# Kernel optimization log

Hardware: AMD Instinct MI355X
Metric: run time of the kernel (lower is better)

## Reference

```python
import jax, jax.numpy as jnp
import numpy as np

N = 100000      # nodes
E = 1600000     # edges
F_IN = 128      # num_feat
H = 128         # hidden_dim
EMB = 64        # node_embedding_dim
HL = 256        # hidden_dim_linear


def setup_inputs() -> dict:
    key = jax.random.key(0)
    ks = jax.random.split(key, 12)
    def w(k, fan_in, shape):
        return jax.random.normal(k, shape, dtype=jnp.float32) / np.sqrt(fan_in)
    x = jax.random.normal(ks[0], (N, F_IN), dtype=jnp.float32)
    edge_index = jax.random.randint(ks[1], (2, E), 0, N, dtype=jnp.int32)
    return {
        "x": x,
        "edge_index": edge_index,
        "W0": w(ks[2], F_IN, (F_IN, H)), "b0": jnp.zeros((H,), jnp.float32),
        "W1": w(ks[3], H, (H, H)),       "b1": jnp.zeros((H,), jnp.float32),
        "W2": w(ks[4], H, (H, EMB)),     "b2": jnp.zeros((EMB,), jnp.float32),
        "lw1": w(ks[5], 2 * EMB, (2 * EMB, HL)), "lb1": jnp.zeros((HL,), jnp.float32),
        "lw2": w(ks[6], HL, (HL, 1)),            "lb2": jnp.zeros((1,), jnp.float32),
    }


def _gcn_forward(x, edge_index, W0, b0, W1, b1, W2, b2, lw1, lb1, lw2, lb2):
    src, dst = edge_index[0], edge_index[1]
    # add self loops (PyG GCNConv default) -- shared across layers
    loop = jnp.arange(N, dtype=src.dtype)
    s = jnp.concatenate([src, loop])
    d = jnp.concatenate([dst, loop])
    # symmetric normalization: deg counts incoming edges incl. self loop (>=1)
    deg = jax.ops.segment_sum(jnp.ones_like(d, dtype=x.dtype), d, num_segments=N)
    norm = jax.lax.rsqrt(deg[s] * deg[d])  # [E+N]

    def conv(h, W, b):
        hw = h @ W                                   # small GEMM [N, out]
        msg = hw[s] * norm[:, None]                  # gather + scale [E+N, out]
        agg = jax.ops.segment_sum(msg, d, num_segments=N)
        return agg + b

    z = jax.nn.relu(conv(x, W0, b0))
    z = jax.nn.relu(conv(z, W1, b1))
    z = jax.nn.relu(conv(z, W2, b2))                 # [N, EMB]  (dropout: eval mode, no-op)

    # edge classifier: gather both endpoints, cat, MLP, sigmoid
    h = jnp.concatenate([z[src], z[dst]], axis=1)    # [E, 2*EMB]
    h = jax.nn.relu(h @ lw1 + lb1)
    return jax.nn.sigmoid(h @ lw2 + lb2)             # [E, 1]


def reference(x, edge_index, W0, b0, W1, b1, W2, b2, lw1, lb1, lw2, lb2):
    return _gcn_forward(x, edge_index, W0, b0, W1, b1, W2, b2, lw1, lb1, lw2, lb2)
```

## Files before the change

### kernel.cpp

```cpp
#include <hip/hip_runtime.h>

#define NNODES 100000
#define NEDGES 1600000
#define NBLK 391
#define NSLICE 8
#define SLICEW 12500
#define CNTB 6250
#define GB0 1563

typedef __attribute__((ext_vector_type(8))) short bf16x8;
typedef __attribute__((ext_vector_type(4))) float f32x4;

__device__ __forceinline__ unsigned short f2bf(float f) {
  unsigned int u = __float_as_uint(f);
  u = (u + 0x7FFFu + ((u >> 16) & 1u)) >> 16;
  return (unsigned short)u;
}
__device__ __forceinline__ float bf2f(unsigned short h) {
  return __uint_as_float(((unsigned int)h) << 16);
}

__device__ __forceinline__ unsigned int pk_add_f16(unsigned int a, unsigned int b) {
  unsigned int r;
  asm("v_pk_add_f16 %0, %1, %2" : "=v"(r) : "v"(a), "v"(b));
  return r;
}
__device__ __forceinline__ unsigned int pk_max0_f16(unsigned int a, unsigned int z) {
  unsigned int r;
  asm("v_pk_max_f16 %0, %1, %2" : "=v"(r) : "v"(a), "v"(z));
  return r;
}
__device__ __forceinline__ float dot2_f16(unsigned int a, unsigned int b, float c) {
  float r;
  asm("v_dot2_f32_f16 %0, %1, %2, %3" : "=v"(r) : "v"(a), "v"(b), "v"(c));
  return r;
}

__global__ __launch_bounds__(256)
void k1_kernel(const int* __restrict__ dst, int* __restrict__ cntD,
               const float* __restrict__ W0, const float* __restrict__ W1,
               const float* __restrict__ W2, const float* __restrict__ lw1,
               const float* __restrict__ lb1, const float* __restrict__ lw2,
               unsigned short* __restrict__ Wp0, unsigned short* __restrict__ Wp1,
               unsigned short* __restrict__ Wp2, unsigned short* __restrict__ WpE,
               float* __restrict__ biasAB, unsigned int* __restrict__ wh) {
  int b = blockIdx.x;
  int tid = threadIdx.x;
  if (b < CNTB) {
    int e = b * 256 + tid;
    if (e < NEDGES) atomicAdd(&cntD[dst[e]], 1);
    return;
  }
  int bb = b - CNTB;
  if (bb < 64) {
    int idx = bb * 256 + tid;
    int k = idx >> 7, c = idx & 127;
    Wp0[((size_t)((k >> 5) * 128 + c)) * 32 + (k & 31)] = f2bf(W0[idx]);
  } else if (bb < 128) {
    int idx = (bb - 64) * 256 + tid;
    int k = idx >> 7, c = idx & 127;
    Wp1[((size_t)((k >> 5) * 128 + c)) * 32 + (k & 31)] = f2bf(W1[idx]);
  } else if (bb < 160) {
    int idx = (bb - 128) * 256 + tid;
    int k = idx >> 6, c = idx & 63;
    Wp2[((size_t)((k >> 5) * 64 + c)) * 32 + (k & 31)] = f2bf(W2[idx]);
  } else {
    int idx = (bb - 160) * 256 + tid;
    int k = idx >> 9, c = idx & 511;
    float v = (c < 256) ? lw1[k * 256 + c] : lw1[(64 + k) * 256 + (c - 256)];
    WpE[((size_t)((k >> 5) * 512 + c)) * 32 + (k & 31)] = f2bf(v);
    if (idx < 512) biasAB[idx] = (idx < 256) ? lb1[idx] : 0.0f;
    if (idx < 128) {
      _Float16 lo = (_Float16)lw2[idx * 2];
      _Float16 hi = (_Float16)lw2[idx * 2 + 1];
      unsigned short ulo = __builtin_bit_cast(unsigned short, lo);
      unsigned short uhi = __builtin_bit_cast(unsigned short, hi);
      wh[idx] = (unsigned int)ulo | ((unsigned int)uhi << 16);
    }
  }
}

__global__ void scanA_kernel(const int* __restrict__ cntD, int* __restrict__ blockSum,
                             float* __restrict__ dis) {
  __shared__ int sh[256];
  int v = blockIdx.x * 256 + threadIdx.x;
  int c = (v < NNODES) ? cntD[v] : 0;
  if (v < NNODES) dis[v] = rsqrtf((float)(c + 1));
  sh[threadIdx.x] = c;
  __syncthreads();
  for (int off = 128; off; off >>= 1) {
    if (threadIdx.x < off) sh[threadIdx.x] += sh[threadIdx.x + off];
    __syncthreads();
  }
  if (threadIdx.x == 0) blockSum[blockIdx.x] = sh[0];
}

__global__ void scanB_kernel(int* __restrict__ blockSum) {
  int lane = threadIdx.x;
  int carry = 0;
  for (int base = 0; base < NBLK; base += 64) {
    int i = base + lane;
    int c = (i < NBLK) ? blockSum[i] : 0;
    int pre = c;
#pragma unroll
    for (int off = 1; off < 64; off <<= 1) {
      int t = __shfl_up(pre, off);
      if (lane >= off) pre += t;
    }
    int tot = __shfl(pre, 63);
    if (i < NBLK) blockSum[i] = carry + pre - c;
    carry += tot;
  }
}

template <int K, int HOUT, bool SCALE, bool BIAS, bool F32IN, bool F16OUT>
__device__ __forceinline__ void mgemm_body(int bid, const void* __restrict__ Xhi_v,
                                           const void* __restrict__ Xlo_v,
                                           const unsigned short* __restrict__ Wp,
                                           const float* __restrict__ dis,
                                           const float* __restrict__ bias,
                                           void* __restrict__ outv) {
  constexpr int KC = K / 32;
  const int tid = threadIdx.x;
  const int wave = tid >> 6;
  const int lane = tid & 63;
  const int lrow = lane & 15;
  const int lsub = lane >> 4;
  const int rowBase = bid * 64 + wave * 16;
  int arow = rowBase + lrow;
  if (arow > NNODES - 1) arow = NNODES - 1;
  bf16x8 ahi[KC], alo[KC];
  if constexpr (F32IN) {
    const float* xf = (const float*)Xhi_v;
#pragma unroll
    for (int kc = 0; kc < KC; ++kc) {
      float4 v0 = *(const float4*)&xf[(size_t)arow * K + kc * 32 + lsub * 8];
      float4 v1 = *(const float4*)&xf[(size_t)arow * K + kc * 32 + lsub * 8 + 4];
      float fv[8] = {v0.x, v0.y, v0.z, v0.w, v1.x, v1.y, v1.z, v1.w};
#pragma unroll
      for (int i = 0; i < 8; ++i) {
        unsigned short h = f2bf(fv[i]);
        ahi[kc][i] = (short)h;
        alo[kc][i] = (short)f2bf(fv[i] - bf2f(h));
      }
    }
  } else {
    const unsigned short* Xhi = (const unsigned short*)Xhi_v;
    const unsigned short* Xlo = (const unsigned short*)Xlo_v;
#pragma unroll
    for (int kc = 0; kc < KC; ++kc) {
      ahi[kc] = *(const bf16x8*)&Xhi[(size_t)arow * K + kc * 32 + lsub * 8];
      alo[kc] = *(const bf16x8*)&Xlo[(size_t)arow * K + kc * 32 + lsub * 8];
    }
  }
  int orow[4];
  float dis4[4];
#pragma unroll
  for (int i = 0; i < 4; ++i) {
    orow[i] = rowBase + lsub * 4 + i;
    int rc = orow[i] < NNODES ? orow[i] : NNODES - 1;
    dis4[i] = SCALE ? dis[rc] : 1.0f;
  }
  for (int ct = 0; ct < HOUT / 16; ++ct) {
    int c = ct * 16 + lrow;
    f32x4 acc = {0.f, 0.f, 0.f, 0.f};
#pragma unroll
    for (int kc = 0; kc < KC; ++kc) {
      bf16x8 b = *(const bf16x8*)&Wp[((size_t)(kc * HOUT + c)) * 32 + lsub * 8];
      acc = __builtin_amdgcn_mfma_f32_16x16x32_bf16(ahi[kc], b, acc, 0, 0, 0);
      acc = __builtin_amdgcn_mfma_f32_16x16x32_bf16(alo[kc], b, acc, 0, 0, 0);
    }
    float bb = BIAS ? bias[c] : 0.0f;
#pragma unroll
    for (int i = 0; i < 4; ++i) {
      if (orow[i] < NNODES) {
        float v = acc[i];
        if (SCALE) v *= dis4[i];
        if (BIAS) v += bb;
        if constexpr (F16OUT) {
          ((_Float16*)outv)[(size_t)orow[i] * HOUT + c] = (_Float16)v;
        } else {
          ((unsigned short*)outv)[(size_t)orow[i] * HOUT + c] = f2bf(v);
        }
      }
    }
  }
}

template <int K, int HOUT, bool SCALE, bool BIAS, bool F32IN, bool F16OUT>
__global__ __launch_bounds__(256)
void mgemm_kernel(const void* __restrict__ Xhi_v, const void* __restrict__ Xlo_v,
                  const unsigned short* __restrict__ Wp, const float* __restrict__ dis,
                  const float* __restrict__ bias, void* __restrict__ outv) {
  mgemm_body<K, HOUT, SCALE, BIAS, F32IN, F16OUT>(blockIdx.x, Xhi_v, Xlo_v, Wp, dis, bias, outv);
}

__global__ __launch_bounds__(256)
void mg0_scanC_kernel(const float* __restrict__ x, const unsigned short* __restrict__ Wp0,
                      const float* __restrict__ dis, unsigned short* __restrict__ P16,
                      const int* __restrict__ cntD, const int* __restrict__ blockSum,
                      int* __restrict__ startD, int* __restrict__ curD) {
  if (blockIdx.x < GB0) {
    mgemm_body<128, 128, true, false, true, false>(blockIdx.x, x, nullptr, Wp0, dis, nullptr, P16);
    return;
  }
  __shared__ int sh[256];
  int bid = blockIdx.x - GB0;
  int tid = threadIdx.x;
  int v = bid * 256 + tid;
  int c = (v < NNODES) ? cntD[v] : 0;
  sh[tid] = c;
  __syncthreads();
  for (int off = 1; off < 256; off <<= 1) {
    int t = (tid >= off) ? sh[tid - off] : 0;
    __syncthreads();
    sh[tid] += t;
    __syncthreads();
  }
  if (v < NNODES) {
    int s = blockSum[bid] + sh[tid] - c;
    startD[v] = s;
    curD[v] = s;
  }
}

__global__ void fill_kernel(const int* __restrict__ src, const int* __restrict__ dst,
                            int* __restrict__ curD, int2* __restrict__ csrPair) {
  int slice = blockIdx.x & (NSLICE - 1);
  int e = (blockIdx.x >> 3) * 256 + threadIdx.x;
  if (e >= NEDGES) return;
  int d = dst[e];
  int lo = slice * SLICEW;
  if (d < lo || d >= lo + SLICEW) return;
  int s = src[e];
  int pd = atomicAdd(&curD[d], 1);
  csrPair[pd] = make_int2(s, e);
}

template <int HOUT>
__global__ __launch_bounds__(256)
void agg_kernel(const unsigned short* __restrict__ hws, const int2* __restrict__ csrPair,
                const int* __restrict__ startA, const int* __restrict__ cnt,
                const float* __restrict__ dis, const float* __restrict__ bias,
                unsigned short* __restrict__ outHi, unsigned short* __restrict__ outLo) {
  int gid = blockIdx.x * 256 + threadIdx.x;
  int v = gid >> 6;
  int lane = gid & 63;
  constexpr int PER = HOUT / 64;
  float acc0 = 0.0f, acc1 = 0.0f;
  if constexpr (PER == 2) {
    unsigned int o = *(const unsigned int*)&hws[(size_t)v * HOUT + lane * 2];
    acc0 = __uint_as_float(o << 16);
    acc1 = __uint_as_float(o & 0xffff0000u);
  } else {
    acc0 = bf2f(hws[(size_t)v * HOUT + lane]);
  }
  int s0 = startA[v], c = cnt[v];
  for (int base = 0; base < c; base += 64) {
    int rem = c - base;
    int m = rem < 64 ? rem : 64;
    int idx = 0;
    if (lane < m) idx = csrPair[s0 + base + lane].x;
    int j = 0;
    for (; j + 8 <= m; j += 8) {
      int u0 = __shfl(idx, j);
      int u1 = __shfl(idx, j + 1);
      int u2 = __shfl(idx, j + 2);
      int u3 = __shfl(idx, j + 3);
      int u4 = __shfl(idx, j + 4);
      int u5 = __shfl(idx, j + 5);
      int u6 = __shfl(idx, j + 6);
      int u7 = __shfl(idx, j + 7);
      if constexpr (PER == 2) {
        unsigned int r0 = *(const unsigned int*)&hws[(size_t)u0 * HOUT + lane * 2];
        unsigned int r1 = *(const unsigned int*)&hws[(size_t)u1 * HOUT + lane * 2];
        unsigned int r2 = *(const unsigned int*)&hws[(size_t)u2 * HOUT + lane * 2];
        unsigned int r3 = *(const unsigned int*)&hws[(size_t)u3 * HOUT + lane * 2];
        unsigned int r4 = *(const unsigned int*)&hws[(size_t)u4 * HOUT + lane * 2];
        unsigned int r5 = *(const unsigned int*)&hws[(size_t)u5 * HOUT + lane * 2];
        unsigned int r6 = *(const unsigned int*)&hws[(size_t)u6 * HOUT + lane * 2];
        unsigned int r7 = *(const unsigned int*)&hws[(size_t)u7 * HOUT + lane * 2];
        acc0 += (__uint_as_float(r0 << 16) + __uint_as_float(r1 << 16)) +
                (__uint_as_float(r2 << 16) + __uint_as_float(r3 << 16)) +
                (__uint_as_float(r4 << 16) + __uint_as_float(r5 << 16)) +
                (__uint_as_float(r6 << 16) + __uint_as_float(r7 << 16));
        acc1 += (__uint_as_float(r0 & 0xffff0000u) + __uint_as_float(r1 & 0xffff0000u)) +
                (__uint_as_float(r2 & 0xffff0000u) + __uint_as_float(r3 & 0xffff0000u)) +
                (__uint_as_float(r4 & 0xffff0000u) + __uint_as_float(r5 & 0xffff0000u)) +
                (__uint_as_float(r6 & 0xffff0000u) + __uint_as_float(r7 & 0xffff0000u));
      } else {
        float r0 = bf2f(hws[(size_t)u0 * HOUT + lane]);
        float r1 = bf2f(hws[(size_t)u1 * HOUT + lane]);
        float r2 = bf2f(hws[(size_t)u2 * HOUT + lane]);
        float r3 = bf2f(hws[(size_t)u3 * HOUT + lane]);
        float r4 = bf2f(hws[(size_t)u4 * HOUT + lane]);
        float r5 = bf2f(hws[(size_t)u5 * HOUT + lane]);
        float r6 = bf2f(hws[(size_t)u6 * HOUT + lane]);
        float r7 = bf2f(hws[(size_t)u7 * HOUT + lane]);
        acc0 += ((r0 + r1) + (r2 + r3)) + ((r4 + r5) + (r6 + r7));
      }
    }
    for (; j + 4 <= m; j += 4) {
      int u0 = __shfl(idx, j);
      int u1 = __shfl(idx, j + 1);
      int u2 = __shfl(idx, j + 2);
      int u3 = __shfl(idx, j + 3);
      if constexpr (PER == 2) {
        unsigned int r0 = *(const unsigned int*)&hws[(size_t)u0 * HOUT + lane * 2];
        unsigned int r1 = *(const unsigned int*)&hws[(size_t)u1 * HOUT + lane * 2];
        unsigned int r2 = *(const unsigned int*)&hws[(size_t)u2 * HOUT + lane * 2];
        unsigned int r3 = *(const unsigned int*)&hws[(size_t)u3 * HOUT + lane * 2];
        acc0 += __uint_as_float(r0 << 16) + __uint_as_float(r1 << 16) +
                __uint_as_float(r2 << 16) + __uint_as_float(r3 << 16);
        acc1 += __uint_as_float(r0 & 0xffff0000u) + __uint_as_float(r1 & 0xffff0000u) +
                __uint_as_float(r2 & 0xffff0000u) + __uint_as_float(r3 & 0xffff0000u);
      } else {
        float r0 = bf2f(hws[(size_t)u0 * HOUT + lane]);
        float r1 = bf2f(hws[(size_t)u1 * HOUT + lane]);
        float r2 = bf2f(hws[(size_t)u2 * HOUT + lane]);
        float r3 = bf2f(hws[(size_t)u3 * HOUT + lane]);
        acc0 += (r0 + r1) + (r2 + r3);
      }
    }
    for (; j < m; ++j) {
      int u = __shfl(idx, j);
      if constexpr (PER == 2) {
        unsigned int r = *(const unsigned int*)&hws[(size_t)u * HOUT + lane * 2];
        acc0 += __uint_as_float(r << 16);
        acc1 += __uint_as_float(r & 0xffff0000u);
      } else {
        acc0 += bf2f(hws[(size_t)u * HOUT + lane]);
      }
    }
  }
  float d = dis[v];
  if constexpr (PER == 2) {
    float o0 = fmaf(d, acc0, bias[lane * 2]);
    float o1 = fmaf(d, acc1, bias[lane * 2 + 1]);
    o0 = o0 > 0.0f ? o0 : 0.0f;
    o1 = o1 > 0.0f ? o1 : 0.0f;
    ushort2 h, l;
    h.x = f2bf(o0); l.x = f2bf(o0 - bf2f(h.x));
    h.y = f2bf(o1); l.y = f2bf(o1 - bf2f(h.y));
    *(ushort2*)&outHi[(size_t)v * HOUT + lane * 2] = h;
    *(ushort2*)&outLo[(size_t)v * HOUT + lane * 2] = l;
  } else {
    float o0 = fmaf(d, acc0, bias[lane]);
    o0 = o0 > 0.0f ? o0 : 0.0f;
    unsigned short h = f2bf(o0);
    outHi[(size_t)v * HOUT + lane] = h;
    outLo[(size_t)v * HOUT + lane] = f2bf(o0 - bf2f(h));
  }
}

__global__ __launch_bounds__(256)
void edge_kernel(const unsigned int* __restrict__ AB32,
                 const int2* __restrict__ csrPair,
                 const int* __restrict__ startD, const int* __restrict__ cntD,
                 const unsigned int* __restrict__ wh, const float* __restrict__ lb2,
                 float* __restrict__ out) {
  int gid = blockIdx.x * 256 + threadIdx.x;
  int v = gid >> 6;
  int lane = gid & 63;
  int sub = lane & 15;
  unsigned int zero = 0u;
  unsigned int bu[8], wu[8];
  {
    const unsigned int* Brow = AB32 + (size_t)v * 256 + 128 + sub * 8;
    uint4 b0 = *(const uint4*)Brow;
    uint4 b1 = *(const uint4*)(Brow + 4);
    bu[0] = b0.x; bu[1] = b0.y; bu[2] = b0.z; bu[3] = b0.w;
    bu[4] = b1.x; bu[5] = b1.y; bu[6] = b1.z; bu[7] = b1.w;
    const unsigned int* W = wh + sub * 8;
    uint4 w0 = *(const uint4*)W;
    uint4 w1 = *(const uint4*)(W + 4);
    wu[0] = w0.x; wu[1] = w0.y; wu[2] = w0.z; wu[3] = w0.w;
    wu[4] = w1.x; wu[5] = w1.y; wu[6] = w1.z; wu[7] = w1.w;
  }
  float lb = lb2[0];

  int s0 = startD[v], c = cntD[v];
  for (int base = 0; base < c; base += 64) {
    int rem = c - base;
    int m = rem < 64 ? rem : 64;
    int sj = 0, ej = 0;
    if (lane < m) {
      int2 p = csrPair[s0 + base + lane];
      sj = p.x; ej = p.y;
    }
    int g = lane >> 4;
    for (int j = 0; j < m; j += 8) {
      int ls0 = j + g, ls1 = j + 4 + g;
      int l0 = ls0 < m ? ls0 : m - 1;
      int l1 = ls1 < m ? ls1 : m - 1;
      int sA = __shfl(sj, l0);
      int eA = __shfl(ej, l0);
      int sB = __shfl(sj, l1);
      int eB = __shfl(ej, l1);
      const unsigned int* ArowA = AB32 + (size_t)(unsigned)sA * 256 + sub * 8;
      const unsigned int* ArowB = AB32 + (size_t)(unsigned)sB * 256 + sub * 8;
      uint4 a00 = *(const uint4*)ArowA;
      uint4 a01 = *(const uint4*)(ArowA + 4);
      uint4 a10 = *(const uint4*)ArowB;
      uint4 a11 = *(const uint4*)(ArowB + 4);
      unsigned int au0[8] = {a00.x, a00.y, a00.z, a00.w, a01.x, a01.y, a01.z, a01.w};
      unsigned int au1[8] = {a10.x, a10.y, a10.z, a10.w, a11.x, a11.y, a11.z, a11.w};
      float acc0 = 0.f, acc1 = 0.f;
#pragma unroll
      for (int i = 0; i < 8; ++i) {
        unsigned int h0 = pk_max0_f16(pk_add_f16(au0[i], bu[i]), zero);
        acc0 = dot2_f16(h0, wu[i], acc0);
        unsigned int h1 = pk_max0_f16(pk_add_f16(au1[i], bu[i]), zero);
        acc1 = dot2_f16(h1, wu[i], acc1);
      }
      acc0 += __shfl_xor(acc0, 1);
      acc0 += __shfl_xor(acc0, 2);
      acc0 += __shfl_xor(acc0, 4);
      acc0 += __shfl_xor(acc0, 8);
      acc1 += __shfl_xor(acc1, 1);
      acc1 += __shfl_xor(acc1, 2);
      acc1 += __shfl_xor(acc1, 4);
      acc1 += __shfl_xor(acc1, 8);
      if (ls0 < m && sub == 0) out[eA] = 1.0f / (1.0f + expf(-(acc0 + lb)));
      if (ls1 < m && sub == 0) out[eB] = 1.0f / (1.0f + expf(-(acc1 + lb)));
    }
  }
}

extern "C" void kernel_launch(void* const* d_in, const int* in_sizes, int n_in,
                              void* d_out, int out_size, void* d_ws, size_t ws_size,
                              hipStream_t stream) {
  const float* x   = (const float*)d_in[0];
  const int*   ei  = (const int*)d_in[1];
  const float* W0  = (const float*)d_in[2];
  const float* b0  = (const float*)d_in[3];
  const float* W1  = (const float*)d_in[4];
  const float* b1  = (const float*)d_in[5];
  const float* W2  = (const float*)d_in[6];
  const float* b2  = (const float*)d_in[7];
  const float* lw1 = (const float*)d_in[8];
  const float* lb1 = (const float*)d_in[9];
  const float* lw2 = (const float*)d_in[10];
  const float* lb2 = (const float*)d_in[11];
  float* out = (float*)d_out;
  const int* src = ei;
  const int* dst = ei + NEDGES;

  char* ws = (char*)d_ws;
  size_t off = 0;
  auto alloc = [&](size_t bytes) -> void* {
    void* p = ws + off;
    off += (bytes + 255) & ~(size_t)255;
    return p;
  };
  int*   cntD   = (int*)alloc((size_t)NNODES * 4);
  int*   startD = (int*)alloc((size_t)NNODES * 4);
  int*   curD   = (int*)alloc((size_t)NNODES * 4);
  float* dis    = (float*)alloc((size_t)NNODES * 4);
  int*   blockSum = (int*)alloc((size_t)NBLK * 4);
  int2*  csrPair= (int2*)alloc((size_t)NEDGES * 8);
  unsigned short* P16  = (unsigned short*)alloc((size_t)NNODES * 128 * 2);
  unsigned short* XQhi = (unsigned short*)alloc((size_t)NNODES * 128 * 2);
  unsigned short* XQlo = (unsigned short*)alloc((size_t)NNODES * 128 * 2);
  void*           AB   = alloc((size_t)NNODES * 512 * 2);
  unsigned short* Wp0  = (unsigned short*)alloc((size_t)128 * 128 * 2);
  unsigned short* Wp1  = (unsigned short*)alloc((size_t)128 * 128 * 2);
  unsigned short* Wp2  = (unsigned short*)alloc((size_t)128 * 64 * 2);
  unsigned short* WpE  = (unsigned short*)alloc((size_t)64 * 512 * 2);
  float* biasAB = (float*)alloc(512 * 4);
  unsigned int* wh = (unsigned int*)alloc(128 * 4);

  const int EB8 = NSLICE * CNTB;
  const int AB_ = (NNODES * 64) / 256;

  hipMemsetAsync(cntD, 0, (size_t)NNODES * 4, stream);
  k1_kernel<<<CNTB + 288, 256, 0, stream>>>(dst, cntD, W0, W1, W2, lw1, lb1, lw2,
                                            Wp0, Wp1, Wp2, WpE, biasAB, wh);
  scanA_kernel<<<NBLK, 256, 0, stream>>>(cntD, blockSum, dis);
  scanB_kernel<<<1, 64, 0, stream>>>(blockSum);
  mg0_scanC_kernel<<<GB0 + NBLK, 256, 0, stream>>>(x, Wp0, dis, P16, cntD, blockSum, startD, curD);
  fill_kernel<<<EB8, 256, 0, stream>>>(src, dst, curD, csrPair);

  agg_kernel<128><<<AB_, 256, 0, stream>>>(P16, csrPair, startD, cntD, dis, b0, XQhi, XQlo);
  mgemm_kernel<128, 128, true, false, false, false><<<GB0, 256, 0, stream>>>(XQhi, XQlo, Wp1, dis, nullptr, P16);
  agg_kernel<128><<<AB_, 256, 0, stream>>>(P16, csrPair, startD, cntD, dis, b1, XQhi, XQlo);
  mgemm_kernel<128, 64, true, false, false, false><<<GB0, 256, 0, stream>>>(XQhi, XQlo, Wp2, dis, nullptr, P16);
  agg_kernel<64><<<AB_, 256, 0, stream>>>(P16, csrPair, startD, cntD, dis, b2, XQhi, XQlo);

  mgemm_kernel<64, 512, false, true, false, true><<<GB0, 256, 0, stream>>>(XQhi, XQlo, WpE, nullptr, biasAB, AB);

  edge_kernel<<<AB_, 256, 0, stream>>>((const unsigned int*)AB, csrPair, startD, cntD, wh, lb2, out);
}
```

Baseline: 580.8 us.

## Fuse neighbor aggregation with following MFMA GEMM via shared-memory staging

Replaces the separate aggregation and GEMM kernels with one fused kernel per layer. Each 64-node block gathers and reduces neighbor features into shared-memory hi/lo bf16 tiles, then runs the MFMA GEMM directly from LDS. This removes the global write and re-read of the intermediate XQhi/XQlo buffers and three kernel launches. In exchange, each wave now handles 16 nodes sequentially instead of one node per wave, which may reduce latency hiding for the irregular gathers and adds LDS pressure that can lower occupancy.

```diff
diff --git a/kernel.cpp b/kernel.cpp
--- a/kernel.cpp
+++ b/kernel.cpp
@@ -113,6 +113,101 @@
   }
 }
 
+template <int H>
+__device__ __forceinline__ void agg_node(int v, const unsigned short* __restrict__ hws,
+                                         const int2* __restrict__ csrPair,
+                                         const int* __restrict__ startD,
+                                         const int* __restrict__ cntD,
+                                         int lane, float& acc0, float& acc1) {
+  constexpr int PER = H / 64;
+  if constexpr (PER == 2) {
+    unsigned int o = *(const unsigned int*)&hws[(size_t)v * H + lane * 2];
+    acc0 = __uint_as_float(o << 16);
+    acc1 = __uint_as_float(o & 0xffff0000u);
+  } else {
+    acc0 = bf2f(hws[(size_t)v * H + lane]);
+    acc1 = 0.0f;
+  }
+  int s0 = startD[v], c = cntD[v];
+  for (int base = 0; base < c; base += 64) {
+    int rem = c - base;
+    int m = rem < 64 ? rem : 64;
+    int idx = 0;
+    if (lane < m) idx = csrPair[s0 + base + lane].x;
+    int j = 0;
+    for (; j + 8 <= m; j += 8) {
+      int u0 = __shfl(idx, j);
+      int u1 = __shfl(idx, j + 1);
+      int u2 = __shfl(idx, j + 2);
+      int u3 = __shfl(idx, j + 3);
+      int u4 = __shfl(idx, j + 4);
+      int u5 = __shfl(idx, j + 5);
+      int u6 = __shfl(idx, j + 6);
+      int u7 = __shfl(idx, j + 7);
+      if constexpr (PER == 2) {
+        unsigned int r0 = *(const unsigned int*)&hws[(size_t)u0 * H + lane * 2];
+        unsigned int r1 = *(const unsigned int*)&hws[(size_t)u1 * H + lane * 2];
+        unsigned int r2 = *(const unsigned int*)&hws[(size_t)u2 * H + lane * 2];
+        unsigned int r3 = *(const unsigned int*)&hws[(size_t)u3 * H + lane * 2];
+        unsigned int r4 = *(const unsigned int*)&hws[(size_t)u4 * H + lane * 2];
+        unsigned int r5 = *(const unsigned int*)&hws[(size_t)u5 * H + lane * 2];
+        unsigned int r6 = *(const unsigned int*)&hws[(size_t)u6 * H + lane * 2];
+        unsigned int r7 = *(const unsigned int*)&hws[(size_t)u7 * H + lane * 2];
+        acc0 += (__uint_as_float(r0 << 16) + __uint_as_float(r1 << 16)) +
+                (__uint_as_float(r2 << 16) + __uint_as_float(r3 << 16)) +
+                (__uint_as_float(r4 << 16) + __uint_as_float(r5 << 16)) +
+                (__uint_as_float(r6 << 16) + __uint_as_float(r7 << 16));
+        acc1 += (__uint_as_float(r0 & 0xffff0000u) + __uint_as_float(r1 & 0xffff0000u)) +
+                (__uint_as_float(r2 & 0xffff0000u) + __uint_as_float(r3 & 0xffff0000u)) +
+                (__uint_as_float(r4 & 0xffff0000u) + __uint_as_float(r5 & 0xffff0000u)) +
+                (__uint_as_float(r6 & 0xffff0000u) + __uint_as_float(r7 & 0xffff0000u));
+      } else {
+        float r0 = bf2f(hws[(size_t)u0 * H + lane]);
+        float r1 = bf2f(hws[(size_t)u1 * H + lane]);
+        float r2 = bf2f(hws[(size_t)u2 * H + lane]);
+        float r3 = bf2f(hws[(size_t)u3 * H + lane]);
+        float r4 = bf2f(hws[(size_t)u4 * H + lane]);
+        float r5 = bf2f(hws[(size_t)u5 * H + lane]);
+        float r6 = bf2f(hws[(size_t)u6 * H + lane]);
+        float r7 = bf2f(hws[(size_t)u7 * H + lane]);
+        acc0 += ((r0 + r1) + (r2 + r3)) + ((r4 + r5) + (r6 + r7));
+      }
+    }
+    for (; j + 4 <= m; j += 4) {
+      int u0 = __shfl(idx, j);
+      int u1 = __shfl(idx, j + 1);
+      int u2 = __shfl(idx, j + 2);
+      int u3 = __shfl(idx, j + 3);
+      if constexpr (PER == 2) {
+        unsigned int r0 = *(const unsigned int*)&hws[(size_t)u0 * H + lane * 2];
+        unsigned int r1 = *(const unsigned int*)&hws[(size_t)u1 * H + lane * 2];
+        unsigned int r2 = *(const unsigned int*)&hws[(size_t)u2 * H + lane * 2];
+        unsigned int r3 = *(const unsigned int*)&hws[(size_t)u3 * H + lane * 2];
+        acc0 += __uint_as_float(r0 << 16) + __uint_as_float(r1 << 16) +
+                __uint_as_float(r2 << 16) + __uint_as_float(r3 << 16);
+        acc1 += __uint_as_float(r0 & 0xffff0000u) + __uint_as_float(r1 & 0xffff0000u) +
+                __uint_as_float(r2 & 0xffff0000u) + __uint_as_float(r3 & 0xffff0000u);
+      } else {
+        float r0 = bf2f(hws[(size_t)u0 * H + lane]);
+        float r1 = bf2f(hws[(size_t)u1 * H + lane]);
+        float r2 = bf2f(hws[(size_t)u2 * H + lane]);
+        float r3 = bf2f(hws[(size_t)u3 * H + lane]);
+        acc0 += (r0 + r1) + (r2 + r3);
+      }
+    }
+    for (; j < m; ++j) {
+      int u = __shfl(idx, j);
+      if constexpr (PER == 2) {
+        unsigned int r = *(const unsigned int*)&hws[(size_t)u * H + lane * 2];
+        acc0 += __uint_as_float(r << 16);
+        acc1 += __uint_as_float(r & 0xffff0000u);
+      } else {
+        acc0 += bf2f(hws[(size_t)u * H + lane]);
+      }
+    }
+  }
+}
+
 template <int K, int HOUT, bool SCALE, bool BIAS, bool F32IN, bool F16OUT>
 __device__ __forceinline__ void mgemm_body(int bid, const void* __restrict__ Xhi_v,
                                            const void* __restrict__ Xlo_v,
@@ -187,14 +282,6 @@
   }
 }
 
-template <int K, int HOUT, bool SCALE, bool BIAS, bool F32IN, bool F16OUT>
-__global__ __launch_bounds__(256)
-void mgemm_kernel(const void* __restrict__ Xhi_v, const void* __restrict__ Xlo_v,
-                  const unsigned short* __restrict__ Wp, const float* __restrict__ dis,
-                  const float* __restrict__ bias, void* __restrict__ outv) {
-  mgemm_body<K, HOUT, SCALE, BIAS, F32IN, F16OUT>(blockIdx.x, Xhi_v, Xlo_v, Wp, dis, bias, outv);
-}
-
 __global__ __launch_bounds__(256)
 void mg0_scanC_kernel(const float* __restrict__ x, const unsigned short* __restrict__ Wp0,
                       const float* __restrict__ dis, unsigned short* __restrict__ P16,
@@ -237,119 +324,90 @@
   csrPair[pd] = make_int2(s, e);
 }
 
-template <int HOUT>
+template <int H, int HOUT2, bool SCALE2, bool BIAS2, bool F16OUT2>
 __global__ __launch_bounds__(256)
-void agg_kernel(const unsigned short* __restrict__ hws, const int2* __restrict__ csrPair,
-                const int* __restrict__ startA, const int* __restrict__ cnt,
-                const float* __restrict__ dis, const float* __restrict__ bias,
-                unsigned short* __restrict__ outHi, unsigned short* __restrict__ outLo) {
-  int gid = blockIdx.x * 256 + threadIdx.x;
-  int v = gid >> 6;
-  int lane = gid & 63;
-  constexpr int PER = HOUT / 64;
-  float acc0 = 0.0f, acc1 = 0.0f;
-  if constexpr (PER == 2) {
-    unsigned int o = *(const unsigned int*)&hws[(size_t)v * HOUT + lane * 2];
-    acc0 = __uint_as_float(o << 16);
-    acc1 = __uint_as_float(o & 0xffff0000u);
-  } else {
-    acc0 = bf2f(hws[(size_t)v * HOUT + lane]);
-  }
-  int s0 = startA[v], c = cnt[v];
-  for (int base = 0; base < c; base += 64) {
-    int rem = c - base;
-    int m = rem < 64 ? rem : 64;
-    int idx = 0;
-    if (lane < m) idx = csrPair[s0 + base + lane].x;
-    int j = 0;
-    for (; j + 8 <= m; j += 8) {
-      int u0 = __shfl(idx, j);
-      int u1 = __shfl(idx, j + 1);
-      int u2 = __shfl(idx, j + 2);
-      int u3 = __shfl(idx, j + 3);
-      int u4 = __shfl(idx, j + 4);
-      int u5 = __shfl(idx, j + 5);
-      int u6 = __shfl(idx, j + 6);
-      int u7 = __shfl(idx, j + 7);
-      if constexpr (PER == 2) {
-        unsigned int r0 = *(const unsigned int*)&hws[(size_t)u0 * HOUT + lane * 2];
-        unsigned int r1 = *(const unsigned int*)&hws[(size_t)u1 * HOUT + lane * 2];
-        unsigned int r2 = *(const unsigned int*)&hws[(size_t)u2 * HOUT + lane * 2];
-        unsigned int r3 = *(const unsigned int*)&hws[(size_t)u3 * HOUT + lane * 2];
-        unsigned int r4 = *(const unsigned int*)&hws[(size_t)u4 * HOUT + lane * 2];
-        unsigned int r5 = *(const unsigned int*)&hws[(size_t)u5 * HOUT + lane * 2];
-        unsigned int r6 = *(const unsigned int*)&hws[(size_t)u6 * HOUT + lane * 2];
-        unsigned int r7 = *(const unsigned int*)&hws[(size_t)u7 * HOUT + lane * 2];
-        acc0 += (__uint_as_float(r0 << 16) + __uint_as_float(r1 << 16)) +
-                (__uint_as_float(r2 << 16) + __uint_as_float(r3 << 16)) +
-                (__uint_as_float(r4 << 16) + __uint_as_float(r5 << 16)) +
-                (__uint_as_float(r6 << 16) + __uint_as_float(r7 << 16));
-        acc1 += (__uint_as_float(r0 & 0xffff0000u) + __uint_as_float(r1 & 0xffff0000u)) +
-                (__uint_as_float(r2 & 0xffff0000u) + __uint_as_float(r3 & 0xffff0000u)) +
-                (__uint_as_float(r4 & 0xffff0000u) + __uint_as_float(r5 & 0xffff0000u)) +
-                (__uint_as_float(r6 & 0xffff0000u) + __uint_as_float(r7 & 0xffff0000u));
-      } else {
-        float r0 = bf2f(hws[(size_t)u0 * HOUT + lane]);
-        float r1 = bf2f(hws[(size_t)u1 * HOUT + lane]);
-        float r2 = bf2f(hws[(size_t)u2 * HOUT + lane]);
-        float r3 = bf2f(hws[(size_t)u3 * HOUT + lane]);
-        float r4 = bf2f(hws[(size_t)u4 * HOUT + lane]);
-        float r5 = bf2f(hws[(size_t)u5 * HOUT + lane]);
-        float r6 = bf2f(hws[(size_t)u6 * HOUT + lane]);
-        float r7 = bf2f(hws[(size_t)u7 * HOUT + lane]);
-        acc0 += ((r0 + r1) + (r2 + r3)) + ((r4 + r5) + (r6 + r7));
-      }
-    }
-    for (; j + 4 <= m; j += 4) {
-      int u0 = __shfl(idx, j);
-      int u1 = __shfl(idx, j + 1);
-      int u2 = __shfl(idx, j + 2);
-      int u3 = __shfl(idx, j + 3);
-      if constexpr (PER == 2) {
-        unsigned int r0 = *(const unsigned int*)&hws[(size_t)u0 * HOUT + lane * 2];
-        unsigned int r1 = *(const unsigned int*)&hws[(size_t)u1 * HOUT + lane * 2];
-        unsigned int r2 = *(const unsigned int*)&hws[(size_t)u2 * HOUT + lane * 2];
-        unsigned int r3 = *(const unsigned int*)&hws[(size_t)u3 * HOUT + lane * 2];
-        acc0 += __uint_as_float(r0 << 16) + __uint_as_float(r1 << 16) +
-                __uint_as_float(r2 << 16) + __uint_as_float(r3 << 16);
-        acc1 += __uint_as_float(r0 & 0xffff0000u) + __uint_as_float(r1 & 0xffff0000u) +
-                __uint_as_float(r2 & 0xffff0000u) + __uint_as_float(r3 & 0xffff0000u);
-      } else {
-        float r0 = bf2f(hws[(size_t)u0 * HOUT + lane]);
-        float r1 = bf2f(hws[(size_t)u1 * HOUT + lane]);
-        float r2 = bf2f(hws[(size_t)u2 * HOUT + lane]);
-        float r3 = bf2f(hws[(size_t)u3 * HOUT + lane]);
-        acc0 += (r0 + r1) + (r2 + r3);
-      }
-    }
-    for (; j < m; ++j) {
-      int u = __shfl(idx, j);
-      if constexpr (PER == 2) {
-        unsigned int r = *(const unsigned int*)&hws[(size_t)u * HOUT + lane * 2];
-        acc0 += __uint_as_float(r << 16);
-        acc1 += __uint_as_float(r & 0xffff0000u);
-      } else {
-        acc0 += bf2f(hws[(size_t)u * HOUT + lane]);
-      }
-    }
-  }
-  float d = dis[v];
-  if constexpr (PER == 2) {
-    float o0 = fmaf(d, acc0, bias[lane * 2]);
-    float o1 = fmaf(d, acc1, bias[lane * 2 + 1]);
-    o0 = o0 > 0.0f ? o0 : 0.0f;
-    o1 = o1 > 0.0f ? o1 : 0.0f;
-    ushort2 h, l;
-    h.x = f2bf(o0); l.x = f2bf(o0 - bf2f(h.x));
-    h.y = f2bf(o1); l.y = f2bf(o1 - bf2f(h.y));
-    *(ushort2*)&outHi[(size_t)v * HOUT + lane * 2] = h;
-    *(ushort2*)&outLo[(size_t)v * HOUT + lane * 2] = l;
-  } else {
-    float o0 = fmaf(d, acc0, bias[lane]);
-    o0 = o0 > 0.0f ? o0 : 0.0f;
-    unsigned short h = f2bf(o0);
-    outHi[(size_t)v * HOUT + lane] = h;
-    outLo[(size_t)v * HOUT + lane] = f2bf(o0 - bf2f(h));
+void fused_kernel(const unsigned short* __restrict__ hws, const int2* __restrict__ csrPair,
+                  const int* __restrict__ startD, const int* __restrict__ cntD,
+                  const float* __restrict__ dis, const float* __restrict__ biasAgg,
+                  const unsigned short* __restrict__ Wp, const float* __restrict__ biasG,
+                  void* __restrict__ outv) {
+  constexpr int PER = H / 64;
+  constexpr int STRIDE = H + 8;
+  constexpr int KC = H / 32;
+  __shared__ unsigned short zhi[64 * STRIDE];
+  __shared__ unsigned short zlo[64 * STRIDE];
+  const int tid = threadIdx.x;
+  const int wave = tid >> 6;
+  const int lane = tid & 63;
+  const int rowBase = blockIdx.x * 64;
+
+  for (int i = 0; i < 16; ++i) {
+    int lr = wave * 16 + i;
+    int v = rowBase + lr;
+    if (v >= NNODES) v = NNODES - 1;
+    float acc0, acc1;
+    agg_node<H>(v, hws, csrPair, startD, cntD, lane, acc0, acc1);
+    float d = dis[v];
+    if constexpr (PER == 2) {
+      float o0 = fmaf(d, acc0, biasAgg[lane * 2]);
+      float o1 = fmaf(d, acc1, biasAgg[lane * 2 + 1]);
+      o0 = o0 > 0.0f ? o0 : 0.0f;
+      o1 = o1 > 0.0f ? o1 : 0.0f;
+      ushort2 h, l;
+      h.x = f2bf(o0); l.x = f2bf(o0 - bf2f(h.x));
+      h.y = f2bf(o1); l.y = f2bf(o1 - bf2f(h.y));
+      *(ushort2*)&zhi[lr * STRIDE + lane * 2] = h;
+      *(ushort2*)&zlo[lr * STRIDE + lane * 2] = l;
+    } else {
+      float o0 = fmaf(d, acc0, biasAgg[lane]);
+      o0 = o0 > 0.0f ? o0 : 0.0f;
+      unsigned short h = f2bf(o0);
+      zhi[lr * STRIDE + lane] = h;
+      zlo[lr * STRIDE + lane] = f2bf(o0 - bf2f(h));
+    }
+  }
+  __syncthreads();
+
+  const int lrow = lane & 15;
+  const int lsub = lane >> 4;
+  const int lr = wave * 16 + lrow;
+  bf16x8 ahi[KC], alo[KC];
+#pragma unroll
+  for (int kc = 0; kc < KC; ++kc) {
+    ahi[kc] = *(const bf16x8*)&zhi[lr * STRIDE + kc * 32 + lsub * 8];
+    alo[kc] = *(const bf16x8*)&zlo[lr * STRIDE + kc * 32 + lsub * 8];
+  }
+  int orow[4];
+  float dis4[4];
+#pragma unroll
+  for (int i = 0; i < 4; ++i) {
+    orow[i] = rowBase + wave * 16 + lsub * 4 + i;
+    int rc = orow[i] < NNODES ? orow[i] : NNODES - 1;
+    dis4[i] = SCALE2 ? dis[rc] : 1.0f;
+  }
+  for (int ct = 0; ct < HOUT2 / 16; ++ct) {
+    int c = ct * 16 + lrow;
+    f32x4 acc = {0.f, 0.f, 0.f, 0.f};
+#pragma unroll
+    for (int kc = 0; kc < KC; ++kc) {
+      bf16x8 b = *(const bf16x8*)&Wp[((size_t)(kc * HOUT2 + c)) * 32 + lsub * 8];
+      acc = __builtin_amdgcn_mfma_f32_16x16x32_bf16(ahi[kc], b, acc, 0, 0, 0);
+      acc = __builtin_amdgcn_mfma_f32_16x16x32_bf16(alo[kc], b, acc, 0, 0, 0);
+    }
+    float bb = BIAS2 ? biasG[c] : 0.0f;
+#pragma unroll
+    for (int i = 0; i < 4; ++i) {
+      if (orow[i] < NNODES) {
+        float v = acc[i];
+        if (SCALE2) v *= dis4[i];
+        if (BIAS2) v += bb;
+        if constexpr (F16OUT2) {
+          ((_Float16*)outv)[(size_t)orow[i] * HOUT2 + c] = (_Float16)v;
+        } else {
+          ((unsigned short*)outv)[(size_t)orow[i] * HOUT2 + c] = f2bf(v);
+        }
+      }
+    }
   }
 }
 
@@ -459,9 +517,8 @@
   float* dis    = (float*)alloc((size_t)NNODES * 4);
   int*   blockSum = (int*)alloc((size_t)NBLK * 4);
   int2*  csrPair= (int2*)alloc((size_t)NEDGES * 8);
-  unsigned short* P16  = (unsigned short*)alloc((size_t)NNODES * 128 * 2);
-  unsigned short* XQhi = (unsigned short*)alloc((size_t)NNODES * 128 * 2);
-  unsigned short* XQlo = (unsigned short*)alloc((size_t)NNODES * 128 * 2);
+  unsigned short* P16a = (unsigned short*)alloc((size_t)NNODES * 128 * 2);
+  unsigned short* P16b = (unsigned short*)alloc((size_t)NNODES * 128 * 2);
   void*           AB   = alloc((size_t)NNODES * 512 * 2);
   unsigned short* Wp0  = (unsigned short*)alloc((size_t)128 * 128 * 2);
   unsigned short* Wp1  = (unsigned short*)alloc((size_t)128 * 128 * 2);
@@ -478,16 +535,15 @@
                                             Wp0, Wp1, Wp2, WpE, biasAB, wh);
   scanA_kernel<<<NBLK, 256, 0, stream>>>(cntD, blockSum, dis);
   scanB_kernel<<<1, 64, 0, stream>>>(blockSum);
-  mg0_scanC_kernel<<<GB0 + NBLK, 256, 0, stream>>>(x, Wp0, dis, P16, cntD, blockSum, startD, curD);
+  mg0_scanC_kernel<<<GB0 + NBLK, 256, 0, stream>>>(x, Wp0, dis, P16a, cntD, blockSum, startD, curD);
   fill_kernel<<<EB8, 256, 0, stream>>>(src, dst, curD, csrPair);
 
-  agg_kernel<128><<<AB_, 256, 0, stream>>>(P16, csrPair, startD, cntD, dis, b0, XQhi, XQlo);
-  mgemm_kernel<128, 128, true, false, false, false><<<GB0, 256, 0, stream>>>(XQhi, XQlo, Wp1, dis, nullptr, P16);
-  agg_kernel<128><<<AB_, 256, 0, stream>>>(P16, csrPair, startD, cntD, dis, b1, XQhi, XQlo);
-  mgemm_kernel<128, 64, true, false, false, false><<<GB0, 256, 0, stream>>>(XQhi, XQlo, Wp2, dis, nullptr, P16);
-  agg_kernel<64><<<AB_, 256, 0, stream>>>(P16, csrPair, startD, cntD, dis, b2, XQhi, XQlo);
-
-  mgemm_kernel<64, 512, false, true, false, true><<<GB0, 256, 0, stream>>>(XQhi, XQlo, WpE, nullptr, biasAB, AB);
+  fused_kernel<128, 128, true, false, false><<<GB0, 256, 0, stream>>>(
+      P16a, csrPair, startD, cntD, dis, b0, Wp1, nullptr, P16b);
+  fused_kernel<128, 64, true, false, false><<<GB0, 256, 0, stream>>>(
+      P16b, csrPair, startD, cntD, dis, b1, Wp2, nullptr, P16a);
+  fused_kernel<64, 512, false, true, true><<<GB0, 256, 0, stream>>>(
+      P16a, csrPair, startD, cntD, dis, b2, WpE, biasAB, AB);
 
   edge_kernel<<<AB_, 256, 0, stream>>>((const unsigned int*)AB, csrPair, startD, cntD, wh, lb2, out);
 }
```

New measurement: 611.1 us. +5.2%, slower.
